# Optimization experiments

Measured on AMD Instinct MI355X. Metric: run time of the kernel, lower is better.

## Reference

```python
import jax, jax.numpy as jnp
import numpy as np

EPS = 1e-8


def setup_inputs() -> dict:
    key = jax.random.key(0)
    k1, k2 = jax.random.split(key)
    latent = jax.random.normal(k1, (16, 192, 64, 64), dtype=jnp.float32)
    codebook = jax.random.normal(k2, (1024, 192), dtype=jnp.float32)
    # codebook rows are unit-normalized at init in the original module
    codebook = codebook / jnp.linalg.norm(codebook, axis=-1, keepdims=True)
    return {"latent": latent, "codebook": codebook}


def reference(latent, codebook):
    b, c, h, w = latent.shape
    # [B,C,H,W] -> [N, C]
    x = jnp.transpose(latent, (0, 2, 3, 1)).reshape(-1, c)
    x = x / (jnp.linalg.norm(x, axis=-1, keepdims=True) + EPS)
    x2 = jnp.sum(x * x, axis=-1, keepdims=True)            # [N,1]
    c2 = jnp.sum(codebook * codebook, axis=-1)             # [K]
    dist_sq = x2 - 2.0 * jnp.einsum('nd,kd->nk', x, codebook) + c2[None, :]
    indices = jnp.argmin(dist_sq, axis=-1)                 # [N]
    quantized_flat = codebook[indices]                     # [N,C] gather
    quantized = jnp.transpose(quantized_flat.reshape(b, h, w, c), (0, 3, 1, 2))
    return quantized, indices.reshape(b, h, w)
```

## Files before the change

### kernel.cpp

```cpp
#include <hip/hip_runtime.h>


#define NPTS   65536
#define DIMS   192
#define KCB    1024
#define HW     4096
#define QELEMS 12582912

typedef __attribute__((ext_vector_type(8))) _Float16 f16x8;
typedef __attribute__((ext_vector_type(4))) _Float16 f16x4;
typedef __attribute__((ext_vector_type(4))) float f32x4;


__device__ __forceinline__ void async_load16(const void* g, void* l) {
    __builtin_amdgcn_global_load_lds(
        (const __attribute__((address_space(1))) unsigned int*)g,
        (__attribute__((address_space(3))) unsigned int*)l, 16, 0, 0);
}

__device__ __forceinline__ void top3_ins(unsigned& b, unsigned& s, unsigned& t,
                                         unsigned p) {
    unsigned m1 = min(b, p);
    unsigned m2 = min(s, p);
    b = max(b, p);
    s = max(s, m1);
    t = max(t, m2);
}

__global__ __launch_bounds__(256) void k_prep(const float* __restrict__ cbk,
                                              _Float16* __restrict__ Bpf,
                                              float* __restrict__ cbkT,
                                              float* __restrict__ c2) {
    __shared__ float q[64 * 193];
    const int tid = threadIdx.x;
    const int k0 = blockIdx.x * 64;
    const int lane = tid & 63;
    const int grp = tid >> 6;
    for (int r = grp; r < 64; r += 4) {
        const float* row = cbk + (size_t)(k0 + r) * DIMS;
        for (int c = lane; c < DIMS; c += 64) q[r * 193 + c] = row[c];
    }
    __syncthreads();
    for (int d = grp; d < DIMS; d += 4)
        cbkT[(size_t)d * KCB + k0 + lane] = q[lane * 193 + d];
    for (int r = grp; r < 64; r += 4)
        for (int c = lane; c < DIMS; c += 64)
            Bpf[((size_t)(c >> 6) * KCB + k0 + r) * 64 + (c & 63)] =
                (_Float16)q[r * 193 + c];
    if (tid < 64) {
        float s = 0.f;
        #pragma unroll 4
        for (int c = 0; c < DIMS; ++c) {
            float v = q[tid * 193 + c];
            s = fmaf(v, v, s);
        }
        c2[k0 + tid] = s;
    }
}

__global__ __launch_bounds__(256, 2) void k_gemm_f(const float* __restrict__ latent,
                                                   const _Float16* __restrict__ Bpf,
                                                   const float* __restrict__ cbkT,
                                                   const float* __restrict__ c2,
                                                   const float* __restrict__ cbk,
                                                   float* __restrict__ out_q,
                                                   float* __restrict__ idxf) {
    __shared__ __align__(16) _Float16 As[128 * 200];
    __shared__ __align__(16) _Float16 Bs[128 * 64];
    __shared__ float nrm_s[128];
    __shared__ uint4 t2buf[256];
    __shared__ int sidx[128];
    __shared__ int slist_pair[128];
    __shared__ int slist_full[128];
    __shared__ int scnt_pair, scnt_full;
    __shared__ float part16[16][16];
    __shared__ float inv16[16];
    __shared__ unsigned long long best16[16];

    const int tid = threadIdx.x;
    const int wave = tid >> 6;
    const int lane = tid & 63;
    const int quad = lane >> 4;
    const int l15 = lane & 15;
    const int wm = (wave >> 1) * 64;
    const int wn = (wave & 1) * 64;
    const int n0 = blockIdx.x * 128;
    const int bB = n0 >> 12;
    const int hw0 = n0 & 4095;
    const size_t latb = (size_t)bB * DIMS * HW;

    {
        float* part = (float*)Bs;
        const float* lat = latent + latb + hw0;
        const int p = tid & 127, ch = tid >> 7;
        float ss = 0.f;
        #pragma unroll 4
        for (int i = 0; i < 24; ++i) {
            int c0 = i * 8 + ch * 4;
            float v0 = lat[(size_t)(c0 + 0) * HW + p];
            float v1 = lat[(size_t)(c0 + 1) * HW + p];
            float v2 = lat[(size_t)(c0 + 2) * HW + p];
            float v3 = lat[(size_t)(c0 + 3) * HW + p];
            ss = fmaf(v0, v0, fmaf(v1, v1, fmaf(v2, v2, fmaf(v3, v3, ss))));
            f16x4 h = { (_Float16)v0, (_Float16)v1, (_Float16)v2, (_Float16)v3 };
            *(f16x4*)&As[p * 200 + c0] = h;
        }
        part[ch * 128 + p] = ss;
        __syncthreads();
        if (tid < 128)
            nrm_s[tid] = sqrtf(part[tid] + part[128 + tid]);
        if (tid == 0) { scnt_pair = 0; scnt_full = 0; }
        __syncthreads();
    }

    unsigned rb[16], rs[16], rt[16];
    #pragma unroll
    for (int i = 0; i < 16; ++i) { rb[i] = 0u; rs[i] = 0u; rt[i] = 0u; }

    for (int nb = 0; nb < 8; ++nb) {
        f32x4 acc[4][4];
        #pragma unroll
        for (int mt = 0; mt < 4; ++mt)
            #pragma unroll
            for (int nt = 0; nt < 4; ++nt)
                #pragma unroll
                for (int r = 0; r < 4; ++r) acc[mt][nt][r] = 0.f;

        for (int g = 0; g < 3; ++g) {
            __syncthreads();
            #pragma unroll
            for (int i = 0; i < 4; ++i) {
                int u = i * 256 + tid;
                int m = u >> 3, c = u & 7;
                int sw = c ^ (m & 7);
                async_load16(Bpf + (((size_t)g * KCB + nb * 128 + m) * 8 + sw) * 8,
                             &Bs[u * 8]);
            }
            asm volatile("s_waitcnt vmcnt(0)" ::: "memory");
            __syncthreads();
            #pragma unroll
            for (int s = 0; s < 2; ++s) {
                f16x8 af[4], bfr[4];
                #pragma unroll
                for (int mt = 0; mt < 4; ++mt) {
                    int m = wm + mt * 16 + l15;
                    af[mt] = *(const f16x8*)&As[m * 200 + g * 64 + s * 32 + quad * 8];
                }
                #pragma unroll
                for (int nt = 0; nt < 4; ++nt) {
                    int n = wn + nt * 16 + l15;
                    int c = (s * 4 + quad) ^ (n & 7);
                    bfr[nt] = *(const f16x8*)&Bs[n * 64 + c * 8];
                }
                #pragma unroll
                for (int mt = 0; mt < 4; ++mt)
                    #pragma unroll
                    for (int nt = 0; nt < 4; ++nt)
                        acc[mt][nt] = __builtin_amdgcn_mfma_f32_16x16x32_f16(
                            af[mt], bfr[nt], acc[mt][nt], 0, 0, 0);
            }
        }

        int kbase = nb * 128 + wn;
        #pragma unroll
        for (int mt = 0; mt < 4; ++mt) {
            #pragma unroll
            for (int r = 0; r < 4; ++r) {
                const int i = mt * 4 + r;
                #pragma unroll
                for (int nt = 0; nt < 4; ++nt) {
                    unsigned pv = ((unsigned)fmaf(acc[mt][nt][r], 65536.f, 2097152.f) << 10)
                                  | (unsigned)(kbase + nt * 16 + l15);
                    top3_ins(rb[i], rs[i], rt[i], pv);
                }
            }
        }
    }

    __syncthreads();
    #pragma unroll
    for (int i = 0; i < 16; ++i) {
        unsigned b = rb[i], s = rs[i], t = rt[i];
        #pragma unroll
        for (int off = 1; off < 16; off <<= 1) {
            unsigned ob = __shfl_xor(b, off, 64);
            unsigned os = __shfl_xor(s, off, 64);
            unsigned ot = __shfl_xor(t, off, 64);
            top3_ins(b, s, t, ob);
            top3_ins(b, s, t, os);
            top3_ins(b, s, t, ot);
        }
        if (l15 == 0) {
            int mt = i >> 2, r = i & 3;
            int mloc = wm + mt * 16 + quad * 4 + r;
            t2buf[mloc * 2 + (wave & 1)] = make_uint4(b, s, t, 0u);
        }
    }
    __syncthreads();
    if (tid < 128) {
        uint4 x = t2buf[tid * 2];
        uint4 y = t2buf[tid * 2 + 1];
        unsigned b = x.x, s = x.y, t = x.z;
        top3_ins(b, s, t, y.x);
        top3_ins(b, s, t, y.y);
        top3_ins(b, s, t, y.z);
        sidx[tid] = (int)(b & 1023u);
        unsigned q1 = b >> 10, q2 = s >> 10, q3 = t >> 10;
        unsigned Mq = (unsigned)fmaf(152.0f, nrm_s[tid], 4.0f);
        if (q1 - q3 < Mq) {
            int pos = atomicAdd(&scnt_full, 1);
            slist_full[pos] = tid;
        } else if (q1 - q2 < Mq) {
            int pos = atomicAdd(&scnt_pair, 1);
            slist_pair[pos] = tid | ((int)(b & 1023u) << 7)
                                  | ((int)(s & 1023u) << 17);
        }
    }
    __syncthreads();
    const int nfull = scnt_full;
    const int npair = scnt_pair;

    {
        float* xsf = (float*)As;
        const float4* ct = (const float4*)cbkT;
        const int j = tid >> 4, dl = tid & 15;
        for (int base = 0; base < nfull; base += 16) {
            const bool valid = (base + j) < nfull;
            const int ploc = valid ? slist_full[base + j] : 0;
            float ss = 0.f;
            if (valid) {
                #pragma unroll
                for (int i = 0; i < 12; ++i) {
                    int d = dl + i * 16;
                    float v = latent[latb + (size_t)d * HW + hw0 + ploc];
                    xsf[j * 200 + d] = v;
                    ss = fmaf(v, v, ss);
                }
            }
            part16[j][dl] = ss;
            if (tid < 16) best16[tid] = ~0ull;
            __syncthreads();
            if (tid < 16) {
                float s = 0.f;
                #pragma unroll
                for (int i = 0; i < 16; ++i) s += part16[tid][i];
                inv16[tid] = 1.0f / (sqrtf(s) + 1e-8f);
            }
            __syncthreads();
            float4 a[16];
            #pragma unroll
            for (int p = 0; p < 16; ++p) a[p] = make_float4(0.f, 0.f, 0.f, 0.f);
            for (int d = 0; d < DIMS; d += 4) {
                float4 cv0 = ct[(size_t)(d + 0) * 256 + tid];
                float4 cv1 = ct[(size_t)(d + 1) * 256 + tid];
                float4 cv2 = ct[(size_t)(d + 2) * 256 + tid];
                float4 cv3 = ct[(size_t)(d + 3) * 256 + tid];
                #pragma unroll
                for (int p = 0; p < 16; ++p) {
                    float4 xv = *(const float4*)&xsf[p * 200 + d];
                    a[p].x = fmaf(xv.x, cv0.x, a[p].x); a[p].y = fmaf(xv.x, cv0.y, a[p].y);
                    a[p].z = fmaf(xv.x, cv0.z, a[p].z); a[p].w = fmaf(xv.x, cv0.w, a[p].w);
                    a[p].x = fmaf(xv.y, cv1.x, a[p].x); a[p].y = fmaf(xv.y, cv1.y, a[p].y);
                    a[p].z = fmaf(xv.y, cv1.z, a[p].z); a[p].w = fmaf(xv.y, cv1.w, a[p].w);
                    a[p].x = fmaf(xv.z, cv2.x, a[p].x); a[p].y = fmaf(xv.z, cv2.y, a[p].y);
                    a[p].z = fmaf(xv.z, cv2.z, a[p].z); a[p].w = fmaf(xv.z, cv2.w, a[p].w);
                    a[p].x = fmaf(xv.w, cv3.x, a[p].x); a[p].y = fmaf(xv.w, cv3.y, a[p].y);
                    a[p].z = fmaf(xv.w, cv3.z, a[p].z); a[p].w = fmaf(xv.w, cv3.w, a[p].w);
                }
            }
            #pragma unroll
            for (int p = 0; p < 16; ++p) {
                float inv = inv16[p];
                float dot4[4] = {a[p].x, a[p].y, a[p].z, a[p].w};
                unsigned long long loc = ~0ull;
                #pragma unroll
                for (int e = 0; e < 4; ++e) {
                    int k = 4 * tid + e;
                    float dist = c2[k] - 2.f * inv * dot4[e];
                    unsigned ub = __float_as_uint(dist);
                    ub ^= (ub >> 31) ? 0xFFFFFFFFu : 0x80000000u;
                    unsigned long long pk =
                        ((unsigned long long)ub << 32) | (unsigned)k;
                    loc = loc < pk ? loc : pk;
                }
                #pragma unroll
                for (int off = 1; off < 64; off <<= 1) {
                    unsigned long long o = __shfl_xor(loc, off, 64);
                    loc = loc < o ? loc : o;
                }
                if ((tid & 63) == 0) atomicMin(&best16[p], loc);
            }
            __syncthreads();
            if (valid && dl == 0)
                sidx[ploc] = (int)(best16[j] & 0xFFFFFFFFull);
            __syncthreads();
        }
    }

    for (int i = tid; i < npair; i += 256) {
        int pk = slist_pair[i];
        int ploc = pk & 127;
        int k1 = (pk >> 7) & 1023;
        int k2 = (pk >> 17) & 1023;
        const float* xr = latent + latb + hw0 + ploc;
        const float* c1 = cbk + (size_t)k1 * DIMS;
        const float* c2r = cbk + (size_t)k2 * DIMS;
        float a1 = 0.f, a2 = 0.f;
        float pp[16];
        #pragma unroll
        for (int e = 0; e < 16; ++e) pp[e] = 0.f;
        for (int d0 = 0; d0 < DIMS; d0 += 16) {
            #pragma unroll
            for (int e = 0; e < 16; ++e) {
                int d = d0 + e;
                float xv = xr[(size_t)d * HW];
                a1 = fmaf(xv, c1[d], a1);
                a2 = fmaf(xv, c2r[d], a2);
                pp[e] = fmaf(xv, xv, pp[e]);
            }
        }
        float ss = 0.f;
        #pragma unroll
        for (int e = 0; e < 16; ++e) ss += pp[e];
        float inv = 1.0f / (sqrtf(ss) + 1e-8f);
        float d1 = c2[k1] - 2.f * inv * a1;
        float d2 = c2[k2] - 2.f * inv * a2;
        unsigned u1 = __float_as_uint(d1);
        u1 ^= (u1 >> 31) ? 0xFFFFFFFFu : 0x80000000u;
        unsigned u2 = __float_as_uint(d2);
        u2 ^= (u2 >> 31) ? 0xFFFFFFFFu : 0x80000000u;
        unsigned long long p1 = ((unsigned long long)u1 << 32) | (unsigned)k1;
        unsigned long long p2 = ((unsigned long long)u2 << 32) | (unsigned)k2;
        sidx[ploc] = (int)((p1 < p2 ? p1 : p2) & 1023ull);
    }
    __syncthreads();

    if (tid < 128) idxf[n0 + tid] = (float)sidx[tid];
    __syncthreads();

    float* q = (float*)As;
    for (int chk = 0; chk < 4; ++chk) {
        int p0 = chk * 32;
        for (int r = wave; r < 32; r += 4) {
            const float* row = cbk + (size_t)sidx[p0 + r] * DIMS;
            for (int c = lane; c < DIMS; c += 64) q[r * 193 + c] = row[c];
        }
        __syncthreads();
        float* ob = out_q + latb + hw0 + p0;
        #pragma unroll
        for (int i = 0; i < 24; ++i) {
            int u = i * 256 + tid;
            int c = u >> 5, p = u & 31;
            ob[(size_t)c * HW + p] = q[p * 193 + c];
        }
        __syncthreads();
    }
}

__global__ __launch_bounds__(256) void k_norms_fb(const float* __restrict__ latent,
                                                  float* __restrict__ inv_norm) {
    __shared__ float red[256];
    const int tid = threadIdx.x;
    const int n0 = blockIdx.x * 128;
    const int nl = tid & 127;
    const int half = tid >> 7;
    const int b = n0 >> 12;
    const int hw = (n0 & 4095) + nl;
    const float* base = latent + (size_t)b * DIMS * HW + hw;
    float ssq = 0.f;
    for (int c = half; c < DIMS; c += 2) {
        float v = base[(size_t)c * HW];
        ssq = fmaf(v, v, ssq);
    }
    red[tid] = ssq;
    __syncthreads();
    if (half == 0) {
        float s = red[tid] + red[tid + 128];
        inv_norm[n0 + nl] = 1.0f / (sqrtf(s) + 1e-8f);
    }
}

__global__ __launch_bounds__(256) void k_c2_fb(const float* __restrict__ cbk,
                                               float* __restrict__ c2) {
    int k = blockIdx.x * 256 + threadIdx.x;
    if (k >= KCB) return;
    const float4* row = (const float4*)(cbk + (size_t)k * DIMS);
    float s = 0.f;
    #pragma unroll
    for (int i = 0; i < DIMS / 4; ++i) {
        float4 v = row[i];
        s += v.x * v.x + v.y * v.y + v.z * v.z + v.w * v.w;
    }
    c2[k] = s;
}

#define LDX  132
__global__ __launch_bounds__(256) void k_dist_fb(const float* __restrict__ latent,
                                                 const float* __restrict__ cbk,
                                                 const float* __restrict__ inv_norm,
                                                 const float* __restrict__ c2,
                                                 int* __restrict__ idx_out,
                                                 float* __restrict__ idxf_out) {
    __shared__ __align__(16) float xsm[64 * LDX];
    __shared__ __align__(16) float csm[64 * LDX];
    __shared__ unsigned long long red[128];
    const int tid = threadIdx.x;
    const int n0 = blockIdx.x * 128;
    const int b = n0 >> 12;
    const int hw0 = n0 & 4095;
    const int kt = tid & 15;
    const int mt = tid >> 4;
    const float* lat_base = latent + (size_t)b * DIMS * HW + hw0;
    float inv[8];
    #pragma unroll
    for (int i = 0; i < 8; ++i) inv[i] = inv_norm[n0 + mt * 8 + i];
    float best[8];
    int bidx[8];
    #pragma unroll
    for (int i = 0; i < 8; ++i) { best[i] = 3.4e38f; bidx[i] = 0; }
    const int nl = tid & 127;
    const int cp = tid >> 7;
    for (int k0 = 0; k0 < KCB; k0 += 128) {
        float acc[8][8];
        #pragma unroll
        for (int i = 0; i < 8; ++i)
            #pragma unroll
            for (int j = 0; j < 8; ++j) acc[i][j] = 0.f;
        for (int d0 = 0; d0 < DIMS; d0 += 64) {
            __syncthreads();
            for (int cc = cp; cc < 64; cc += 2)
                xsm[cc * LDX + nl] = lat_base[(size_t)(d0 + cc) * HW + nl];
            #pragma unroll
            for (int i = 0; i < 8; ++i) {
                int f4 = tid + 256 * i;
                int kk = f4 >> 4;
                int dq = f4 & 15;
                float4 v = *(const float4*)(cbk + (size_t)(k0 + kk) * DIMS + d0 + dq * 4);
                csm[(dq * 4 + 0) * LDX + kk] = v.x;
                csm[(dq * 4 + 1) * LDX + kk] = v.y;
                csm[(dq * 4 + 2) * LDX + kk] = v.z;
                csm[(dq * 4 + 3) * LDX + kk] = v.w;
            }
            __syncthreads();
            for (int d = 0; d < 64; ++d) {
                const float* xr = &xsm[d * LDX + mt * 8];
                const float* cr = &csm[d * LDX + kt * 8];
                float x8[8], c8[8];
                *(float4*)&x8[0] = *(const float4*)&xr[0];
                *(float4*)&x8[4] = *(const float4*)&xr[4];
                *(float4*)&c8[0] = *(const float4*)&cr[0];
                *(float4*)&c8[4] = *(const float4*)&cr[4];
                #pragma unroll
                for (int i = 0; i < 8; ++i)
                    #pragma unroll
                    for (int j = 0; j < 8; ++j)
                        acc[i][j] = fmaf(x8[i], c8[j], acc[i][j]);
            }
        }
        float cc2[8];
        #pragma unroll
        for (int j = 0; j < 8; ++j) cc2[j] = c2[k0 + kt * 8 + j];
        #pragma unroll
        for (int i = 0; i < 8; ++i)
            #pragma unroll
            for (int j = 0; j < 8; ++j) {
                float t = inv[i] * acc[i][j];
                float dist = fmaf(-2.f, t, cc2[j]);
                int kidx = k0 + kt * 8 + j;
                if (dist < best[i]) { best[i] = dist; bidx[i] = kidx; }
            }
    }
    if (tid < 128) red[tid] = ~0ull;
    __syncthreads();
    #pragma unroll
    for (int i = 0; i < 8; ++i) {
        unsigned long long p =
            ((unsigned long long)__float_as_uint(best[i]) << 32) | (unsigned)bidx[i];
        atomicMin(&red[mt * 8 + i], p);
    }
    __syncthreads();
    if (tid < 128) {
        int k = (int)(red[tid] & 0xFFFFFFFFu);
        idx_out[n0 + tid] = k;
        idxf_out[n0 + tid] = (float)k;
    }
}

__global__ __launch_bounds__(256) void k_gather(const float* __restrict__ cbk,
                                                const int* __restrict__ idx,
                                                float* __restrict__ out) {
    __shared__ float q[64 * 193];
    __shared__ int sidx[64];
    const int tid = threadIdx.x;
    const int n0 = blockIdx.x * 64;
    const int b = n0 >> 12;
    const int hw0 = n0 & 4095;
    const int lane = tid & 63;
    const int grp = tid >> 6;

    if (tid < 64) sidx[tid] = idx[n0 + tid];
    __syncthreads();
    for (int r = grp; r < 64; r += 4) {
        const float* row = cbk + (size_t)sidx[r] * DIMS;
        for (int c = lane; c < DIMS; c += 64) q[r * 193 + c] = row[c];
    }
    __syncthreads();
    float* obase = out + (size_t)b * DIMS * HW + hw0;
    for (int c = grp; c < DIMS; c += 4) {
        obase[(size_t)c * HW + lane] = q[lane * 193 + c];
    }
}

extern "C" void kernel_launch(void* const* d_in, const int* in_sizes, int n_in,
                              void* d_out, int out_size, void* d_ws, size_t ws_size,
                              hipStream_t stream) {
    const float* latent = (const float*)d_in[0];
    const float* cbk = (const float*)d_in[1];
    float* out = (float*)d_out;
    float* out_q = out;
    float* out_idx = out + QELEMS;

    if (ws_size >= 2u * 1024u * 1024u) {
        char* w = (char*)d_ws;
        _Float16* Bpf = (_Float16*)w;
        float* cbkT = (float*)(w + 393216);
        float* c2 = (float*)(w + 1179648);

        k_prep<<<KCB / 64, 256, 0, stream>>>(cbk, Bpf, cbkT, c2);
        k_gemm_f<<<512, 256, 0, stream>>>(latent, Bpf, cbkT, c2, cbk,
                                          out_q, out_idx);
    } else {
        float* inv_norm = (float*)d_ws;
        float* c2 = inv_norm + NPTS;
        int* idx = (int*)(c2 + KCB);
        k_norms_fb<<<NPTS / 128, 256, 0, stream>>>(latent, inv_norm);
        k_c2_fb<<<4, 256, 0, stream>>>(cbk, c2);
        k_dist_fb<<<NPTS / 128, 256, 0, stream>>>(latent, cbk, inv_norm, c2, idx, out_idx);
        k_gather<<<NPTS / 64, 256, 0, stream>>>(cbk, idx, out_q);
    }
}
```

Measured before the change: 216.5 us.

## Double-buffer codebook tiles in GEMM, shrink prep blocks and rescoring batch

The main GEMM loop now streams the codebook in 32-wide half-slices into two LDS buffers. Each async prefetch is issued before the MFMAs of the current slice, replacing the old load-wait-compute pattern. The same LDS budget gives one barrier per half-slice and a new swizzle. The prep kernel uses 16-row blocks so more blocks run in parallel, and full rescoring batches 8 points instead of 16 to cut per-batch waste when few points need rescoring.

```diff
diff --git a/kernel.cpp b/kernel.cpp
--- a/kernel.cpp
+++ b/kernel.cpp
@@ -31,23 +31,26 @@
                                               _Float16* __restrict__ Bpf,
                                               float* __restrict__ cbkT,
                                               float* __restrict__ c2) {
-    __shared__ float q[64 * 193];
+    __shared__ float q[16 * 193];
     const int tid = threadIdx.x;
-    const int k0 = blockIdx.x * 64;
+    const int k0 = blockIdx.x * 16;
     const int lane = tid & 63;
     const int grp = tid >> 6;
-    for (int r = grp; r < 64; r += 4) {
+    for (int r = grp; r < 16; r += 4) {
         const float* row = cbk + (size_t)(k0 + r) * DIMS;
         for (int c = lane; c < DIMS; c += 64) q[r * 193 + c] = row[c];
     }
     __syncthreads();
-    for (int d = grp; d < DIMS; d += 4)
-        cbkT[(size_t)d * KCB + k0 + lane] = q[lane * 193 + d];
-    for (int r = grp; r < 64; r += 4)
+    {
+        const int kl = tid & 15, dg = tid >> 4;
+        for (int d = dg; d < DIMS; d += 16)
+            cbkT[(size_t)d * KCB + k0 + kl] = q[kl * 193 + d];
+    }
+    for (int r = grp; r < 16; r += 4)
         for (int c = lane; c < DIMS; c += 64)
             Bpf[((size_t)(c >> 6) * KCB + k0 + r) * 64 + (c & 63)] =
                 (_Float16)q[r * 193 + c];
-    if (tid < 64) {
+    if (tid < 16) {
         float s = 0.f;
         #pragma unroll 4
         for (int c = 0; c < DIMS; ++c) {
@@ -66,16 +69,16 @@
                                                    float* __restrict__ out_q,
                                                    float* __restrict__ idxf) {
     __shared__ __align__(16) _Float16 As[128 * 200];
-    __shared__ __align__(16) _Float16 Bs[128 * 64];
+    __shared__ __align__(16) _Float16 Bs[2][4096];
     __shared__ float nrm_s[128];
     __shared__ uint4 t2buf[256];
     __shared__ int sidx[128];
     __shared__ int slist_pair[128];
     __shared__ int slist_full[128];
     __shared__ int scnt_pair, scnt_full;
-    __shared__ float part16[16][16];
-    __shared__ float inv16[16];
-    __shared__ unsigned long long best16[16];
+    __shared__ float part8[8][32];
+    __shared__ float inv8[8];
+    __shared__ unsigned long long best8[8];
 
     const int tid = threadIdx.x;
     const int wave = tid >> 6;
@@ -90,7 +93,7 @@
     const size_t latb = (size_t)bB * DIMS * HW;
 
     {
-        float* part = (float*)Bs;
+        float* part = (float*)&Bs[0][0];
         const float* lat = latent + latb + hw0;
         const int p = tid & 127, ch = tid >> 7;
         float ss = 0.f;
@@ -113,10 +116,18 @@
         __syncthreads();
     }
 
+    const int sk0 = tid >> 2,        sj0 = (tid & 3) ^ ((sk0 >> 1) & 3);
+    const int sk1 = (tid + 256) >> 2, sj1 = ((tid + 256) & 3) ^ ((sk1 >> 1) & 3);
+
+    async_load16(Bpf + ((size_t)sk0) * 64 + sj0 * 8, &Bs[0][tid * 8]);
+    async_load16(Bpf + ((size_t)sk1) * 64 + sj1 * 8, &Bs[0][(tid + 256) * 8]);
+
     unsigned rb[16], rs[16], rt[16];
     #pragma unroll
     for (int i = 0; i < 16; ++i) { rb[i] = 0u; rs[i] = 0u; rt[i] = 0u; }
 
+    int nb_s = 0, h_s = 1;
+
     for (int nb = 0; nb < 8; ++nb) {
         f32x4 acc[4][4];
         #pragma unroll
@@ -126,39 +137,38 @@
                 #pragma unroll
                 for (int r = 0; r < 4; ++r) acc[mt][nt][r] = 0.f;
 
-        for (int g = 0; g < 3; ++g) {
-            __syncthreads();
-            #pragma unroll
-            for (int i = 0; i < 4; ++i) {
-                int u = i * 256 + tid;
-                int m = u >> 3, c = u & 7;
-                int sw = c ^ (m & 7);
-                async_load16(Bpf + (((size_t)g * KCB + nb * 128 + m) * 8 + sw) * 8,
-                             &Bs[u * 8]);
-            }
+        #pragma unroll
+        for (int h = 0; h < 6; ++h) {
+            const int ph = nb * 6 + h;
             asm volatile("s_waitcnt vmcnt(0)" ::: "memory");
             __syncthreads();
-            #pragma unroll
-            for (int s = 0; s < 2; ++s) {
-                f16x8 af[4], bfr[4];
-                #pragma unroll
-                for (int mt = 0; mt < 4; ++mt) {
-                    int m = wm + mt * 16 + l15;
-                    af[mt] = *(const f16x8*)&As[m * 200 + g * 64 + s * 32 + quad * 8];
-                }
-                #pragma unroll
-                for (int nt = 0; nt < 4; ++nt) {
-                    int n = wn + nt * 16 + l15;
-                    int c = (s * 4 + quad) ^ (n & 7);
-                    bfr[nt] = *(const f16x8*)&Bs[n * 64 + c * 8];
-                }
-                #pragma unroll
-                for (int mt = 0; mt < 4; ++mt)
-                    #pragma unroll
-                    for (int nt = 0; nt < 4; ++nt)
-                        acc[mt][nt] = __builtin_amdgcn_mfma_f32_16x16x32_f16(
-                            af[mt], bfr[nt], acc[mt][nt], 0, 0, 0);
-            }
+            if (ph < 47) {
+                const size_t gb = ((size_t)(h_s >> 1) * KCB + nb_s * 128) * 64
+                                  + (h_s & 1) * 32;
+                async_load16(Bpf + gb + (size_t)sk0 * 64 + sj0 * 8,
+                             &Bs[(ph + 1) & 1][tid * 8]);
+                async_load16(Bpf + gb + (size_t)sk1 * 64 + sj1 * 8,
+                             &Bs[(ph + 1) & 1][(tid + 256) * 8]);
+                if (++h_s == 6) { h_s = 0; ++nb_s; }
+            }
+            const int g = h >> 1, s = h & 1;
+            f16x8 af[4], bfr[4];
+            #pragma unroll
+            for (int mt = 0; mt < 4; ++mt) {
+                int m = wm + mt * 16 + l15;
+                af[mt] = *(const f16x8*)&As[m * 200 + g * 64 + s * 32 + quad * 8];
+            }
+            #pragma unroll
+            for (int nt = 0; nt < 4; ++nt) {
+                int n = wn + nt * 16 + l15;
+                bfr[nt] = *(const f16x8*)&Bs[ph & 1][n * 32 + (quad ^ ((n >> 1) & 3)) * 8];
+            }
+            #pragma unroll
+            for (int mt = 0; mt < 4; ++mt)
+                #pragma unroll
+                for (int nt = 0; nt < 4; ++nt)
+                    acc[mt][nt] = __builtin_amdgcn_mfma_f32_16x16x32_f16(
+                        af[mt], bfr[nt], acc[mt][nt], 0, 0, 0);
         }
 
         int kbase = nb * 128 + wn;
@@ -223,40 +233,40 @@
     {
         float* xsf = (float*)As;
         const float4* ct = (const float4*)cbkT;
-        const int j = tid >> 4, dl = tid & 15;
-        for (int base = 0; base < nfull; base += 16) {
-            const bool valid = (base + j) < nfull;
-            const int ploc = valid ? slist_full[base + j] : 0;
+        const int j8 = tid >> 5, dl = tid & 31;
+        for (int base = 0; base < nfull; base += 8) {
+            const bool valid = (base + j8) < nfull;
+            const int ploc = valid ? slist_full[base + j8] : 0;
             float ss = 0.f;
             if (valid) {
                 #pragma unroll
-                for (int i = 0; i < 12; ++i) {
-                    int d = dl + i * 16;
+                for (int i = 0; i < 6; ++i) {
+                    int d = dl + i * 32;
                     float v = latent[latb + (size_t)d * HW + hw0 + ploc];
-                    xsf[j * 200 + d] = v;
+                    xsf[j8 * 200 + d] = v;
                     ss = fmaf(v, v, ss);
                 }
             }
-            part16[j][dl] = ss;
-            if (tid < 16) best16[tid] = ~0ull;
-            __syncthreads();
-            if (tid < 16) {
+            part8[j8][dl] = ss;
+            if (tid < 8) best8[tid] = ~0ull;
+            __syncthreads();
+            if (tid < 8) {
                 float s = 0.f;
                 #pragma unroll
-                for (int i = 0; i < 16; ++i) s += part16[tid][i];
-                inv16[tid] = 1.0f / (sqrtf(s) + 1e-8f);
-            }
-            __syncthreads();
-            float4 a[16];
-            #pragma unroll
-            for (int p = 0; p < 16; ++p) a[p] = make_float4(0.f, 0.f, 0.f, 0.f);
+                for (int i = 0; i < 32; ++i) s += part8[tid][i];
+                inv8[tid] = 1.0f / (sqrtf(s) + 1e-8f);
+            }
+            __syncthreads();
+            float4 a[8];
+            #pragma unroll
+            for (int p = 0; p < 8; ++p) a[p] = make_float4(0.f, 0.f, 0.f, 0.f);
             for (int d = 0; d < DIMS; d += 4) {
                 float4 cv0 = ct[(size_t)(d + 0) * 256 + tid];
                 float4 cv1 = ct[(size_t)(d + 1) * 256 + tid];
                 float4 cv2 = ct[(size_t)(d + 2) * 256 + tid];
                 float4 cv3 = ct[(size_t)(d + 3) * 256 + tid];
                 #pragma unroll
-                for (int p = 0; p < 16; ++p) {
+                for (int p = 0; p < 8; ++p) {
                     float4 xv = *(const float4*)&xsf[p * 200 + d];
                     a[p].x = fmaf(xv.x, cv0.x, a[p].x); a[p].y = fmaf(xv.x, cv0.y, a[p].y);
                     a[p].z = fmaf(xv.x, cv0.z, a[p].z); a[p].w = fmaf(xv.x, cv0.w, a[p].w);
@@ -269,8 +279,8 @@
                 }
             }
             #pragma unroll
-            for (int p = 0; p < 16; ++p) {
-                float inv = inv16[p];
+            for (int p = 0; p < 8; ++p) {
+                float inv = inv8[p];
                 float dot4[4] = {a[p].x, a[p].y, a[p].z, a[p].w};
                 unsigned long long loc = ~0ull;
                 #pragma unroll
@@ -288,11 +298,11 @@
                     unsigned long long o = __shfl_xor(loc, off, 64);
                     loc = loc < o ? loc : o;
                 }
-                if ((tid & 63) == 0) atomicMin(&best16[p], loc);
+                if ((tid & 63) == 0) atomicMin(&best8[p], loc);
             }
             __syncthreads();
             if (valid && dl == 0)
-                sidx[ploc] = (int)(best16[j] & 0xFFFFFFFFull);
+                sidx[ploc] = (int)(best8[j8] & 0xFFFFFFFFull);
             __syncthreads();
         }
     }
@@ -526,7 +536,7 @@
         float* cbkT = (float*)(w + 393216);
         float* c2 = (float*)(w + 1179648);
 
-        k_prep<<<KCB / 64, 256, 0, stream>>>(cbk, Bpf, cbkT, c2);
+        k_prep<<<KCB / 16, 256, 0, stream>>>(cbk, Bpf, cbkT, c2);
         k_gemm_f<<<512, 256, 0, stream>>>(latent, Bpf, cbkT, c2, cbk,
                                           out_q, out_idx);
     } else {
```

Result: faster. 194.9 us (-10.0%).
